# Kernel optimization log

Hardware: AMD Instinct MI355X
Metric: run time of the kernel (lower is better)

## Reference

```python
import jax, jax.numpy as jnp
import numpy as np

B, L, D_MODEL, H = 4, 4096, 1024, 16
HD = D_MODEL // H
EPS = 1e-6


def setup_inputs() -> dict:
    key = jax.random.key(0)
    ks = jax.random.split(key, 5)
    s = 1.0 / np.sqrt(D_MODEL)
    return {
        "x": jax.random.normal(ks[0], (B, L, D_MODEL), dtype=jnp.float32),
        "Wq": jax.random.normal(ks[1], (D_MODEL, D_MODEL), dtype=jnp.float32) * s,
        "bq": jnp.zeros((D_MODEL,), jnp.float32),
        "Wk": jax.random.normal(ks[2], (D_MODEL, D_MODEL), dtype=jnp.float32) * s,
        "bk": jnp.zeros((D_MODEL,), jnp.float32),
        "Wv": jax.random.normal(ks[3], (D_MODEL, D_MODEL), dtype=jnp.float32) * s,
        "bv": jnp.zeros((D_MODEL,), jnp.float32),
        "Wo": jax.random.normal(ks[4], (D_MODEL, D_MODEL), dtype=jnp.float32) * s,
        "bo": jnp.zeros((D_MODEL,), jnp.float32),
    }


def _heads(y):
    # (B, L, d_model) -> (B, H, L, head_dim)
    b, l, _ = y.shape
    return jnp.transpose(y.reshape(b, l, H, HD), (0, 2, 1, 3))


def reference(x, Wq, bq, Wk, bk, Wv, bv, Wo, bo):
    b, l, _ = x.shape
    q = jax.nn.sigmoid(_heads(x @ Wq + bq))  # kernel feature map
    k = jax.nn.sigmoid(_heads(x @ Wk + bk))
    v = _heads(x @ Wv + bv)

    sink_incoming = 1.0 / jnp.einsum('bhld,bhd->bhl', q + EPS, k.sum(axis=2) + EPS)
    source_outgoing = 1.0 / jnp.einsum('bhld,bhd->bhl', k + EPS, q.sum(axis=2) + EPS)
    conserved_sink = jnp.einsum(
        'bhld,bhd->bhl', q + EPS,
        (k * source_outgoing[..., None]).sum(axis=2) + EPS)
    conserved_source = jnp.einsum(
        'bhld,bhd->bhl', k + EPS,
        (q * sink_incoming[..., None]).sum(axis=2) + EPS)
    conserved_source = jnp.clip(conserved_source, -1.0, 1.0)

    sink_allocation = jax.nn.sigmoid(conserved_sink * (float(l) / float(l)))
    source_competition = jax.nn.softmax(conserved_source, axis=-1) * float(l)

    # linear attention: kv state (B,H,HD,HD) then apply to queries
    kv = jnp.einsum('bhld,bhlm->bhdm', k, v * source_competition[..., None])
    out = jnp.einsum('bhld,bhdm->bhlm', q * sink_incoming[..., None], kv)
    out = out * sink_allocation[..., None]

    out = jnp.transpose(out, (0, 2, 1, 3)).reshape(b, l, D_MODEL)
    # dropout is identity at inference
    return out @ Wo + bo
```

## Files before the change

### kernel.cpp

```cpp
#include <hip/hip_runtime.h>
#include <hip/hip_bf16.h>
#include <stdint.h>

#define SEQ    4096
#define DMODEL 1024
#define NHEAD  16
#define HDIM   64
#define NBATCH 4
#define NBH    (NBATCH*NHEAD)
#define MTOK   (NBATCH*SEQ)
#define FEPS   1e-6f
#define PLANE  16777216u

typedef float f32x4 __attribute__((ext_vector_type(4)));
typedef short bf16x8 __attribute__((ext_vector_type(8)));

#define XB_OFF    0u
#define WQKV_OFF  33554432u
#define WO_OFF    39845888u
#define QKV_OFF   41943040u
#define AOB_OFF   142606336u
#define ST_OFF    176160768u
#define KSUM_OFF  (ST_OFF)
#define QSUM_OFF  (ST_OFF + 16384u)
#define QSI_OFF   (ST_OFF + 32768u)
#define KSO_OFF   (ST_OFF + 49152u)
#define ESUM_OFF  (ST_OFF + 65536u)
#define SI_OFF    (ST_OFF + 81920u)
#define SA_OFF    (SI_OFF + 1048576u)
#define KVF_OFF   (SA_OFF + 1048576u)
#define KVP_OFF   (KVF_OFF + 1048576u)

#define S_VMCNT(N) asm volatile("s_waitcnt vmcnt(" #N ")" ::: "memory")
#define BARRIER() do { __builtin_amdgcn_s_barrier(); asm volatile("" ::: "memory"); } while (0)

__device__ __forceinline__ unsigned short f2bf(float f) {
  __hip_bfloat16 h = __float2bfloat16(f);
  unsigned short u; __builtin_memcpy(&u, &h, 2); return u;
}
__device__ __forceinline__ float bf2f(unsigned short u) {
  union { unsigned u; float f; } x; x.u = ((unsigned)u) << 16; return x.f;
}
__device__ __forceinline__ void decode8(uint4 r, float* o) {
  o[0] = bf2f((unsigned short)(r.x & 0xffffu)); o[1] = bf2f((unsigned short)(r.x >> 16));
  o[2] = bf2f((unsigned short)(r.y & 0xffffu)); o[3] = bf2f((unsigned short)(r.y >> 16));
  o[4] = bf2f((unsigned short)(r.z & 0xffffu)); o[5] = bf2f((unsigned short)(r.z >> 16));
  o[6] = bf2f((unsigned short)(r.w & 0xffffu)); o[7] = bf2f((unsigned short)(r.w >> 16));
}
__device__ __forceinline__ void gll(const unsigned short* g, unsigned short* l) {
  __builtin_amdgcn_global_load_lds((const __attribute__((address_space(1))) void*)g,
      (__attribute__((address_space(3))) void*)l, 16, 0, 0);
}

__global__ __launch_bounds__(256) void conv_all_k(const float* __restrict__ x,
                                                  const float* __restrict__ Wq, const float* __restrict__ Wk,
                                                  const float* __restrict__ Wv, const float* __restrict__ Wo,
                                                  unsigned short* __restrict__ xb,
                                                  unsigned short* __restrict__ Wqkvt,
                                                  unsigned short* __restrict__ Wot) {
  const int bx = blockIdx.x;
  if (bx < 1024) {
    __shared__ float tile[64][65];
    const int z = bx >> 8, tl = bx & 255;
    const float* W = (z == 0) ? Wq : (z == 1) ? Wk : (z == 2) ? Wv : Wo;
    unsigned short* dst = (z < 3) ? (Wqkvt + (size_t)z * 1024u * 1024u) : Wot;
    const int n0 = (tl & 15) * 64, k0 = (tl >> 4) * 64;
    const int tx = threadIdx.x & 63, ty = threadIdx.x >> 6;
    for (int i = ty; i < 64; i += 4)
      tile[i][tx] = W[(size_t)(k0 + i) * 1024 + n0 + tx];
    __syncthreads();
    for (int i = ty; i < 64; i += 4)
      dst[(size_t)(n0 + i) * 1024 + k0 + tx] = f2bf(tile[tx][i]);
  } else {
    const int n = MTOK * DMODEL;
    int i = ((bx - 1024) * 256 + threadIdx.x) * 4;
    const int stride = (gridDim.x - 1024) * 256 * 4;
    for (; i < n; i += stride) {
      float4 v = *(const float4*)(x + i);
      ushort4 o;
      o.x = f2bf(v.x); o.y = f2bf(v.y); o.z = f2bf(v.z); o.w = f2bf(v.w);
      *(ushort4*)(xb + i) = o;
    }
  }
}

template <int MODE>
__global__ __launch_bounds__(512, 2) void gemm8p(const unsigned short* __restrict__ A,
                                                 const unsigned short* __restrict__ Bt,
                                                 const float* __restrict__ b0,
                                                 const float* __restrict__ b1,
                                                 const float* __restrict__ b2,
                                                 float* __restrict__ qsum_g,
                                                 float* __restrict__ ksum_g,
                                                 void* __restrict__ C, int Ndim) {
  constexpr int Kd = 1024;
  constexpr int NT = Kd >> 6;
  __shared__ unsigned short sm[8 * 8192];
  const int tid = threadIdx.x;
  const int wid = tid >> 6, lane = tid & 63;
  const int wr = wid >> 2, wc = wid & 3;

  const int gx = gridDim.x;
  const int nwg = gx * gridDim.y;
  int wg = blockIdx.y * gx + blockIdx.x;
  wg = (wg & 7) * (nwg >> 3) + (wg >> 3);
  const int n0 = (wg % gx) * 256, m0 = (wg / gx) * 256;

  const int rl = lane & 15, kob = (lane >> 4) << 4;
  const int xs2 = (rl & 7) << 3;
  const int ca0 = (kob >> 1) ^ xs2;
  const int ca1 = (32 + (kob >> 1)) ^ xs2;
  const int brow0 = (wc & 1) * 64;
  const unsigned short* ArA = sm + wr * 8192 + rl * 64 + ca0;
  const unsigned short* ArB = sm + wr * 8192 + rl * 64 + ca1;
  const unsigned short* BrA = sm + (2 + (wc >> 1)) * 8192 + (brow0 + rl) * 64 + ca0;
  const unsigned short* BrB = sm + (2 + (wc >> 1)) * 8192 + (brow0 + rl) * 64 + ca1;

  const int srow = tid >> 3;
  const int scol = (((tid & 7) * 16) ^ ((srow & 7) << 4)) >> 1;
  const unsigned short* gA0 = A + (size_t)(m0 + srow) * Kd + scol;
  const unsigned short* gA1 = gA0 + 64 * Kd;
  const unsigned short* gA2 = gA0 + 128 * Kd;
  const unsigned short* gA3 = gA0 + 192 * Kd;
  const unsigned short* gB0 = Bt + (size_t)(n0 + srow) * Kd + scol;
  const unsigned short* gB1 = gB0 + 64 * Kd;
  const unsigned short* gB2 = gB0 + 128 * Kd;
  const unsigned short* gB3 = gB0 + 192 * Kd;
  unsigned short* ldst = sm + tid * 8;

  f32x4 acc[8][4];
#pragma unroll
  for (int i = 0; i < 8; ++i)
#pragma unroll
    for (int j = 0; j < 4; ++j) acc[i][j] = (f32x4){0.f, 0.f, 0.f, 0.f};

#define STG(g0, g1, R, T) do { \
    gll((g0) + (T) * 64, ldst + (R) * 8192); \
    gll((g1) + (T) * 64, ldst + (R) * 8192 + 4096); } while (0)

  STG(gA0, gA1, 0, 0); STG(gA2, gA3, 1, 0);
  STG(gB0, gB1, 2, 0); STG(gB2, gB3, 3, 0);
  STG(gA0, gA1, 4, 1); STG(gA2, gA3, 5, 1);
  S_VMCNT(4);
  BARRIER();

#define KBODY(U, BUF) do { \
    constexpr int BO = (BUF) * 32768; \
    bf16x8 a0[4][2], a1[4][2], b01[2][2], b23[2][2]; \
    _Pragma("unroll") for (int m = 0; m < 4; ++m) { \
      a0[m][0] = *(const bf16x8*)(ArA + BO + m * 1024); \
      a0[m][1] = *(const bf16x8*)(ArB + BO + m * 1024); } \
    _Pragma("unroll") for (int n = 0; n < 2; ++n) { \
      b01[n][0] = *(const bf16x8*)(BrA + BO + n * 1024); \
      b01[n][1] = *(const bf16x8*)(BrB + BO + n * 1024); } \
    if ((U) + 1 < NT) STG(gB0, gB1, (!(BUF)) * 4 + 2, (U) + 1); \
    BARRIER(); \
    __builtin_amdgcn_s_setprio(1); \
    _Pragma("unroll") for (int m = 0; m < 4; ++m) \
      _Pragma("unroll") for (int n = 0; n < 2; ++n) { \
        acc[m][n] = __builtin_amdgcn_mfma_f32_16x16x32_bf16(a0[m][0], b01[n][0], acc[m][n], 0, 0, 0); \
        acc[m][n] = __builtin_amdgcn_mfma_f32_16x16x32_bf16(a0[m][1], b01[n][1], acc[m][n], 0, 0, 0); } \
    __builtin_amdgcn_s_setprio(0); \
    BARRIER(); \
    _Pragma("unroll") for (int m = 0; m < 4; ++m) { \
      a1[m][0] = *(const bf16x8*)(ArA + BO + 4096 + m * 1024); \
      a1[m][1] = *(const bf16x8*)(ArB + BO + 4096 + m * 1024); } \
    if ((U) + 1 < NT) STG(gB2, gB3, (!(BUF)) * 4 + 3, (U) + 1); \
    BARRIER(); \
    __builtin_amdgcn_s_setprio(1); \
    _Pragma("unroll") for (int m = 0; m < 4; ++m) \
      _Pragma("unroll") for (int n = 0; n < 2; ++n) { \
        acc[4 + m][n] = __builtin_amdgcn_mfma_f32_16x16x32_bf16(a1[m][0], b01[n][0], acc[4 + m][n], 0, 0, 0); \
        acc[4 + m][n] = __builtin_amdgcn_mfma_f32_16x16x32_bf16(a1[m][1], b01[n][1], acc[4 + m][n], 0, 0, 0); } \
    __builtin_amdgcn_s_setprio(0); \
    BARRIER(); \
    _Pragma("unroll") for (int n = 0; n < 2; ++n) { \
      b23[n][0] = *(const bf16x8*)(BrA + BO + (2 + n) * 1024); \
      b23[n][1] = *(const bf16x8*)(BrB + BO + (2 + n) * 1024); } \
    if ((U) + 2 < NT) STG(gA0, gA1, (BUF) * 4, (U) + 2); \
    BARRIER(); \
    __builtin_amdgcn_s_setprio(1); \
    _Pragma("unroll") for (int m = 0; m < 4; ++m) \
      _Pragma("unroll") for (int n = 0; n < 2; ++n) { \
        acc[4 + m][2 + n] = __builtin_amdgcn_mfma_f32_16x16x32_bf16(a1[m][0], b23[n][0], acc[4 + m][2 + n], 0, 0, 0); \
        acc[4 + m][2 + n] = __builtin_amdgcn_mfma_f32_16x16x32_bf16(a1[m][1], b23[n][1], acc[4 + m][2 + n], 0, 0, 0); } \
    __builtin_amdgcn_s_setprio(0); \
    BARRIER(); \
    if ((U) + 2 < NT) STG(gA2, gA3, (BUF) * 4 + 1, (U) + 2); \
    BARRIER(); \
    __builtin_amdgcn_s_setprio(1); \
    _Pragma("unroll") for (int m = 0; m < 4; ++m) \
      _Pragma("unroll") for (int n = 0; n < 2; ++n) { \
        acc[m][2 + n] = __builtin_amdgcn_mfma_f32_16x16x32_bf16(a0[m][0], b23[n][0], acc[m][2 + n], 0, 0, 0); \
        acc[m][2 + n] = __builtin_amdgcn_mfma_f32_16x16x32_bf16(a0[m][1], b23[n][1], acc[m][2 + n], 0, 0, 0); } \
    __builtin_amdgcn_s_setprio(0); \
    if ((U) + 2 < NT) { S_VMCNT(4); } else { S_VMCNT(0); } \
    BARRIER(); \
  } while (0)

  for (int u = 0; u < NT; u += 2) {
    KBODY(u, 0);
    KBODY(u + 1, 1);
  }
#undef KBODY
#undef STG

  const int cr = (lane >> 4) * 4, cc = lane & 15;
  float cs[4] = {0.f, 0.f, 0.f, 0.f};
#pragma unroll
  for (int m = 0; m < 8; ++m)
#pragma unroll
    for (int n = 0; n < 4; ++n)
#pragma unroll
      for (int rr = 0; rr < 4; ++rr) {
        const int gr = m0 + wr * 128 + m * 16 + cr + rr;
        const int gc = n0 + wc * 64 + n * 16 + cc;
        float v = acc[m][n][rr];
        if (MODE == 0) {
          const float bias = (gc < 1024) ? b0[gc] : ((gc < 2048) ? b1[gc - 1024] : b2[gc - 2048]);
          v += bias;
          if (gc < 2048) v = 1.f / (1.f + __expf(-v));
          cs[n] += v;
          const size_t addr = (size_t)(gc >> 10) * PLANE +
                              ((size_t)(((gr >> 12) << 4) | ((gc >> 6) & 15)) * 4096 + (gr & 4095)) * 64 +
                              (gc & 63);
          ((unsigned short*)C)[addr] = f2bf(v);
        } else {
          v += b0[gc];
          ((float*)C)[(size_t)gr * Ndim + gc] = v;
        }
      }
  if (MODE == 0 && n0 < 2048) {
#pragma unroll
    for (int n = 0; n < 4; ++n) {
      cs[n] += __shfl_xor(cs[n], 16);
      cs[n] += __shfl_xor(cs[n], 32);
    }
    if (lane < 16) {
      const int b = m0 >> 12;
#pragma unroll
      for (int n = 0; n < 4; ++n) {
        const int gc = n0 + wc * 64 + n * 16 + lane;
        const int h = (gc & 1023) >> 6, d = gc & 63;
        float* tgt = (gc < 1024) ? qsum_g : ksum_g;
        atomicAdd(&tgt[((b << 4) + h) * 64 + d], cs[n]);
      }
    }
  }
}

__global__ __launch_bounds__(256) void flow1_k(const unsigned short* __restrict__ Qp,
                                               const unsigned short* __restrict__ Kp,
                                               const float* __restrict__ ksum, const float* __restrict__ qsum,
                                               float* __restrict__ si, float* __restrict__ qsi,
                                               float* __restrict__ kso) {
  const int bh = blockIdx.x >> 3, c = blockIdx.x & 7;
  const int w = threadIdx.x >> 6, lane = threadIdx.x & 63;
  const float ks = ksum[bh * 64 + lane] + FEPS;
  const float qs = qsum[bh * 64 + lane] + FEPS;
  const size_t hb = (size_t)bh * 262144 + lane;
  float qsi_acc = 0.f, kso_acc = 0.f;
  const int l0 = c * 512 + w * 128;
  for (int l = l0; l < l0 + 128; l += 4) {
    float qv[4], kvv[4], dq[4], dk[4];
#pragma unroll
    for (int u = 0; u < 4; ++u) {
      const size_t off = hb + (size_t)(l + u) * 64;
      qv[u] = bf2f(Qp[off]);
      kvv[u] = bf2f(Kp[off]);
      dq[u] = (qv[u] + FEPS) * ks;
      dk[u] = (kvv[u] + FEPS) * qs;
    }
#pragma unroll
    for (int m = 1; m < 64; m <<= 1)
#pragma unroll
      for (int u = 0; u < 4; ++u) { dq[u] += __shfl_xor(dq[u], m); dk[u] += __shfl_xor(dk[u], m); }
#pragma unroll
    for (int u = 0; u < 4; ++u) {
      const float siv = 1.f / dq[u], sov = 1.f / dk[u];
      if (lane == 0) si[(size_t)bh * SEQ + l + u] = siv;
      qsi_acc += qv[u] * siv;
      kso_acc += kvv[u] * sov;
    }
  }
  atomicAdd(&qsi[bh * 64 + lane], qsi_acc);
  atomicAdd(&kso[bh * 64 + lane], kso_acc);
}

__global__ __launch_bounds__(256) void flow2kv_k(const unsigned short* __restrict__ Qp,
                                                 const unsigned short* __restrict__ Kp,
                                                 const unsigned short* __restrict__ Vp,
                                                 const float* __restrict__ qsi, const float* __restrict__ kso,
                                                 float* __restrict__ sa, float* __restrict__ esum,
                                                 float* __restrict__ kvp) {
  const int bh = blockIdx.x >> 3, c = blockIdx.x & 7;
  __shared__ float eel[512];
  __shared__ float kch[32][64];
  __shared__ float vch[32][64];
  const int t = threadIdx.x;
  const int w = t >> 6, lane = t & 63;
  const size_t hb = (size_t)bh * 262144;

  {
    const float kov = kso[bh * 64 + lane] + FEPS;
    const float qiv = qsi[bh * 64 + lane] + FEPS;
    const size_t base = hb + lane;
    float es = 0.f;
    const int l0 = c * 512 + w * 128;
    for (int l = l0; l < l0 + 128; l += 4) {
      float ds[4], dr[4];
#pragma unroll
      for (int u = 0; u < 4; ++u) {
        const size_t off = base + (size_t)(l + u) * 64;
        ds[u] = (bf2f(Qp[off]) + FEPS) * kov;
        dr[u] = (bf2f(Kp[off]) + FEPS) * qiv;
      }
#pragma unroll
      for (int m = 1; m < 64; m <<= 1)
#pragma unroll
        for (int u = 0; u < 4; ++u) { ds[u] += __shfl_xor(ds[u], m); dr[u] += __shfl_xor(dr[u], m); }
#pragma unroll
      for (int u = 0; u < 4; ++u) {
        const float sig = 1.f / (1.f + __expf(-ds[u]));
        const float cse = fminf(1.f, fmaxf(-1.f, dr[u]));
        const float e = __expf(cse);
        if (lane == 0) { sa[(size_t)bh * SEQ + l + u] = sig; eel[l - c * 512 + u] = e; }
        es += e;
      }
    }
    if (lane == 0) atomicAdd(&esum[bh], es);
  }
  __syncthreads();

  const int sl = t >> 3, sd = (t & 7) * 8;
  const int d1 = (t >> 4) * 4, d2 = (t & 15) * 4;
  float acc[4][4] = {};
  for (int ch = 0; ch < 16; ++ch) {
    const int lloc = ch * 32 + sl;
    const size_t off = hb + (size_t)(c * 512 + lloc) * 64 + sd;
    const uint4 kr = *(const uint4*)(Kp + off);
    const uint4 vr = *(const uint4*)(Vp + off);
    const float cmp = eel[lloc];
    float kd[8], vd[8];
    decode8(kr, kd); decode8(vr, vd);
    __syncthreads();
    *(f32x4*)&kch[sl][sd]     = (f32x4){kd[0], kd[1], kd[2], kd[3]};
    *(f32x4*)&kch[sl][sd + 4] = (f32x4){kd[4], kd[5], kd[6], kd[7]};
    *(f32x4*)&vch[sl][sd]     = (f32x4){vd[0] * cmp, vd[1] * cmp, vd[2] * cmp, vd[3] * cmp};
    *(f32x4*)&vch[sl][sd + 4] = (f32x4){vd[4] * cmp, vd[5] * cmp, vd[6] * cmp, vd[7] * cmp};
    __syncthreads();
    for (int l = 0; l < 32; ++l) {
      const f32x4 ka = *(const f32x4*)&kch[l][d1];
      const f32x4 vb = *(const f32x4*)&vch[l][d2];
#pragma unroll
      for (int i = 0; i < 4; ++i)
#pragma unroll
        for (int j = 0; j < 4; ++j) acc[i][j] += ka[i] * vb[j];
    }
    __syncthreads();
  }
  float* dst = kvp + (size_t)blockIdx.x * 4096;
#pragma unroll
  for (int i = 0; i < 4; ++i)
    *(f32x4*)&dst[(d1 + i) * 64 + d2] = (f32x4){acc[i][0], acc[i][1], acc[i][2], acc[i][3]};
}

__global__ __launch_bounds__(256) void kvred_k(const float* __restrict__ kvp,
                                               const float* __restrict__ esum,
                                               float* __restrict__ kvf) {
  const int idx = blockIdx.x * 256 + threadIdx.x;
  const int bh = idx >> 12, e = idx & 4095;
  const float Ls = 4096.f / esum[bh];
  float s = 0.f;
#pragma unroll
  for (int cN = 0; cN < 8; ++cN) s += kvp[((size_t)(bh * 8 + cN) << 12) + e];
  kvf[idx] = s * Ls;
}

__global__ __launch_bounds__(256) void outk_k(const unsigned short* __restrict__ Qp,
                                              const float* __restrict__ kvf, const float* __restrict__ si,
                                              const float* __restrict__ sa,
                                              unsigned short* __restrict__ AOb) {
  const int bh = blockIdx.x >> 4, lc = blockIdx.x & 15;
  const int b = bh >> 4, h = bh & 15;
  __shared__ unsigned short kvT[4096];
  const int t = threadIdx.x;
  const int w = t >> 6, lane = t & 63;
  for (int i = t; i < 4096; i += 256) {
    const int dd = i >> 6, d = i & 63;
    kvT[d * 64 + (dd ^ ((d & 7) << 3))] = f2bf(kvf[(size_t)bh * 4096 + i]);
  }
  __syncthreads();

  const int rl = lane & 15, g = lane >> 4;
  const size_t hb = (size_t)bh * 262144;
  const int l0 = lc * 256 + w * 64;

  bf16x8 a[4][2], bf[4][2];
#pragma unroll
  for (int m = 0; m < 4; ++m) {
    const size_t q0 = hb + (size_t)(l0 + m * 16 + rl) * 64 + g * 8;
    a[m][0] = *(const bf16x8*)(Qp + q0);
    a[m][1] = *(const bf16x8*)(Qp + q0 + 32);
  }
#pragma unroll
  for (int n = 0; n < 4; ++n) {
    const int r = n * 16 + rl;
    const int sw = (r & 7) << 3;
    bf[n][0] = *(const bf16x8*)(kvT + r * 64 + ((g * 8) ^ sw));
    bf[n][1] = *(const bf16x8*)(kvT + r * 64 + ((32 + g * 8) ^ sw));
  }
  f32x4 acc[4][4];
#pragma unroll
  for (int i = 0; i < 4; ++i)
#pragma unroll
    for (int j = 0; j < 4; ++j) acc[i][j] = (f32x4){0.f, 0.f, 0.f, 0.f};
#pragma unroll
  for (int m = 0; m < 4; ++m)
#pragma unroll
    for (int n = 0; n < 4; ++n) {
      acc[m][n] = __builtin_amdgcn_mfma_f32_16x16x32_bf16(a[m][0], bf[n][0], acc[m][n], 0, 0, 0);
      acc[m][n] = __builtin_amdgcn_mfma_f32_16x16x32_bf16(a[m][1], bf[n][1], acc[m][n], 0, 0, 0);
    }

  const int cr = (lane >> 4) * 4, cc = lane & 15;
#pragma unroll
  for (int m = 0; m < 4; ++m)
#pragma unroll
    for (int rr = 0; rr < 4; ++rr) {
      const int l = l0 + m * 16 + cr + rr;
      const size_t sidx = (size_t)bh * SEQ + l;
      const float sc = si[sidx] * sa[sidx];
      unsigned short* orow = AOb + (size_t)(b * SEQ + l) * 1024 + h * 64 + cc;
#pragma unroll
      for (int n = 0; n < 4; ++n)
        orow[n * 16] = f2bf(acc[m][n][rr] * sc);
    }
}

extern "C" void kernel_launch(void* const* d_in, const int* in_sizes, int n_in,
                              void* d_out, int out_size, void* d_ws, size_t ws_size,
                              hipStream_t stream) {
  const float* x  = (const float*)d_in[0];
  const float* Wq = (const float*)d_in[1];
  const float* bq = (const float*)d_in[2];
  const float* Wk = (const float*)d_in[3];
  const float* bk = (const float*)d_in[4];
  const float* Wv = (const float*)d_in[5];
  const float* bv = (const float*)d_in[6];
  const float* Wo = (const float*)d_in[7];
  const float* bo = (const float*)d_in[8];
  char* ws = (char*)d_ws;
  unsigned short* Xb    = (unsigned short*)(ws + XB_OFF);
  unsigned short* Wqkvt = (unsigned short*)(ws + WQKV_OFF);
  unsigned short* Wot   = (unsigned short*)(ws + WO_OFF);
  unsigned short* QKV   = (unsigned short*)(ws + QKV_OFF);
  unsigned short* AOb   = (unsigned short*)(ws + AOB_OFF);
  unsigned short* Qp = QKV;
  unsigned short* Kp = QKV + PLANE;
  unsigned short* Vp = QKV + 2 * PLANE;
  float* ksum = (float*)(ws + KSUM_OFF);
  float* qsum = (float*)(ws + QSUM_OFF);
  float* qsi  = (float*)(ws + QSI_OFF);
  float* kso  = (float*)(ws + KSO_OFF);
  float* esum = (float*)(ws + ESUM_OFF);
  float* si   = (float*)(ws + SI_OFF);
  float* sa   = (float*)(ws + SA_OFF);
  float* kvf  = (float*)(ws + KVF_OFF);
  float* kvp  = (float*)(ws + KVP_OFF);

  (void)hipMemsetAsync(ws + ST_OFF, 0, 81920, stream);
  conv_all_k<<<3072, 256, 0, stream>>>(x, Wq, Wk, Wv, Wo, Xb, Wqkvt, Wot);
  gemm8p<0><<<dim3(12, 64), 512, 0, stream>>>(Xb, Wqkvt, bq, bk, bv, qsum, ksum, (void*)QKV, 3072);
  flow1_k<<<NBH * 8, 256, 0, stream>>>(Qp, Kp, ksum, qsum, si, qsi, kso);
  flow2kv_k<<<NBH * 8, 256, 0, stream>>>(Qp, Kp, Vp, qsi, kso, sa, esum, kvp);
  kvred_k<<<1024, 256, 0, stream>>>(kvp, esum, kvf);
  outk_k<<<NBH * 16, 256, 0, stream>>>(Qp, kvf, si, sa, AOb);
  gemm8p<1><<<dim3(4, 64), 512, 0, stream>>>(AOb, Wot, bo, nullptr, nullptr, nullptr, nullptr, d_out, 1024);
}
```

Measured before the change: 335.3 us.

## Vectorize flow kernels' row reductions and fold KV partial reduction into output kernel

flow1_k and the first phase of flow2kv_k now load 8 bf16 values per lane with 16-byte loads, so 8 lanes cover one 64-wide row and each wave processes 8 rows at a time. This replaces scalar 2-byte loads and full 64-lane shuffle reductions with a 3-step shuffle, plus a final cross-row shuffle before the atomics. The separate kvred_k launch is removed. outk_k now sums the 8 KV partials itself and applies the esum scale, which drops one kernel launch and the kvf round trip through memory. The cost is that each of the 16 outk blocks per head repeats the partial-sum work.

```diff
diff --git a/kernel.cpp b/kernel.cpp
--- a/kernel.cpp
+++ b/kernel.cpp
@@ -28,8 +28,7 @@
 #define ESUM_OFF  (ST_OFF + 65536u)
 #define SI_OFF    (ST_OFF + 81920u)
 #define SA_OFF    (SI_OFF + 1048576u)
-#define KVF_OFF   (SA_OFF + 1048576u)
-#define KVP_OFF   (KVF_OFF + 1048576u)
+#define KVP_OFF   (SA_OFF + 1048576u)
 
 #define S_VMCNT(N) asm volatile("s_waitcnt vmcnt(" #N ")" ::: "memory")
 #define BARRIER() do { __builtin_amdgcn_s_barrier(); asm volatile("" ::: "memory"); } while (0)
@@ -255,36 +254,49 @@
                                                float* __restrict__ si, float* __restrict__ qsi,
                                                float* __restrict__ kso) {
   const int bh = blockIdx.x >> 3, c = blockIdx.x & 7;
-  const int w = threadIdx.x >> 6, lane = threadIdx.x & 63;
-  const float ks = ksum[bh * 64 + lane] + FEPS;
-  const float qs = qsum[bh * 64 + lane] + FEPS;
-  const size_t hb = (size_t)bh * 262144 + lane;
-  float qsi_acc = 0.f, kso_acc = 0.f;
-  const int l0 = c * 512 + w * 128;
-  for (int l = l0; l < l0 + 128; l += 4) {
-    float qv[4], kvv[4], dq[4], dk[4];
-#pragma unroll
-    for (int u = 0; u < 4; ++u) {
-      const size_t off = hb + (size_t)(l + u) * 64;
-      qv[u] = bf2f(Qp[off]);
-      kvv[u] = bf2f(Kp[off]);
-      dq[u] = (qv[u] + FEPS) * ks;
-      dk[u] = (kvv[u] + FEPS) * qs;
-    }
-#pragma unroll
-    for (int m = 1; m < 64; m <<= 1)
-#pragma unroll
-      for (int u = 0; u < 4; ++u) { dq[u] += __shfl_xor(dq[u], m); dk[u] += __shfl_xor(dk[u], m); }
-#pragma unroll
-    for (int u = 0; u < 4; ++u) {
-      const float siv = 1.f / dq[u], sov = 1.f / dk[u];
-      if (lane == 0) si[(size_t)bh * SEQ + l + u] = siv;
-      qsi_acc += qv[u] * siv;
-      kso_acc += kvv[u] * sov;
-    }
-  }
-  atomicAdd(&qsi[bh * 64 + lane], qsi_acc);
-  atomicAdd(&kso[bh * 64 + lane], kso_acc);
+  const int t = threadIdx.x;
+  const int w = t >> 6, lane = t & 63;
+  const int r = lane >> 3, dg = lane & 7;
+  const size_t hb = (size_t)bh * 262144;
+  float ksv[8], qsv[8];
+#pragma unroll
+  for (int j = 0; j < 8; ++j) {
+    ksv[j] = ksum[bh * 64 + dg * 8 + j] + FEPS;
+    qsv[j] = qsum[bh * 64 + dg * 8 + j] + FEPS;
+  }
+  float qsi_acc[8] = {}, kso_acc[8] = {};
+  const int l0w = c * 512 + w * 128;
+  for (int l4 = 0; l4 < 128; l4 += 8) {
+    const int l = l0w + l4 + r;
+    const size_t off = hb + (size_t)l * 64 + dg * 8;
+    const uint4 qr = *(const uint4*)(Qp + off);
+    const uint4 kr = *(const uint4*)(Kp + off);
+    float qd[8], kd[8];
+    decode8(qr, qd); decode8(kr, kd);
+    float dq = 0.f, dk = 0.f;
+#pragma unroll
+    for (int j = 0; j < 8; ++j) { dq += (qd[j] + FEPS) * ksv[j]; dk += (kd[j] + FEPS) * qsv[j]; }
+#pragma unroll
+    for (int m = 1; m < 8; m <<= 1) { dq += __shfl_xor(dq, m); dk += __shfl_xor(dk, m); }
+    const float siv = 1.f / dq, sov = 1.f / dk;
+    if (dg == 0) si[(size_t)bh * SEQ + l] = siv;
+#pragma unroll
+    for (int j = 0; j < 8; ++j) { qsi_acc[j] += qd[j] * siv; kso_acc[j] += kd[j] * sov; }
+  }
+#pragma unroll
+  for (int m = 8; m < 64; m <<= 1)
+#pragma unroll
+    for (int j = 0; j < 8; ++j) {
+      qsi_acc[j] += __shfl_xor(qsi_acc[j], m);
+      kso_acc[j] += __shfl_xor(kso_acc[j], m);
+    }
+  if (lane < 8) {
+#pragma unroll
+    for (int j = 0; j < 8; ++j) {
+      atomicAdd(&qsi[bh * 64 + lane * 8 + j], qsi_acc[j]);
+      atomicAdd(&kso[bh * 64 + lane * 8 + j], kso_acc[j]);
+    }
+  }
 }
 
 __global__ __launch_bounds__(256) void flow2kv_k(const unsigned short* __restrict__ Qp,
@@ -302,32 +314,38 @@
   const size_t hb = (size_t)bh * 262144;
 
   {
-    const float kov = kso[bh * 64 + lane] + FEPS;
-    const float qiv = qsi[bh * 64 + lane] + FEPS;
-    const size_t base = hb + lane;
+    const int r = lane >> 3, dg = lane & 7;
+    float kov[8], qiv[8];
+#pragma unroll
+    for (int j = 0; j < 8; ++j) {
+      kov[j] = kso[bh * 64 + dg * 8 + j] + FEPS;
+      qiv[j] = qsi[bh * 64 + dg * 8 + j] + FEPS;
+    }
     float es = 0.f;
-    const int l0 = c * 512 + w * 128;
-    for (int l = l0; l < l0 + 128; l += 4) {
-      float ds[4], dr[4];
-#pragma unroll
-      for (int u = 0; u < 4; ++u) {
-        const size_t off = base + (size_t)(l + u) * 64;
-        ds[u] = (bf2f(Qp[off]) + FEPS) * kov;
-        dr[u] = (bf2f(Kp[off]) + FEPS) * qiv;
-      }
-#pragma unroll
-      for (int m = 1; m < 64; m <<= 1)
-#pragma unroll
-        for (int u = 0; u < 4; ++u) { ds[u] += __shfl_xor(ds[u], m); dr[u] += __shfl_xor(dr[u], m); }
-#pragma unroll
-      for (int u = 0; u < 4; ++u) {
-        const float sig = 1.f / (1.f + __expf(-ds[u]));
-        const float cse = fminf(1.f, fmaxf(-1.f, dr[u]));
-        const float e = __expf(cse);
-        if (lane == 0) { sa[(size_t)bh * SEQ + l + u] = sig; eel[l - c * 512 + u] = e; }
+    const int l0w = c * 512 + w * 128;
+    for (int l4 = 0; l4 < 128; l4 += 8) {
+      const int l = l0w + l4 + r;
+      const size_t off = hb + (size_t)l * 64 + dg * 8;
+      const uint4 qr = *(const uint4*)(Qp + off);
+      const uint4 kr = *(const uint4*)(Kp + off);
+      float qd[8], kd[8];
+      decode8(qr, qd); decode8(kr, kd);
+      float ds = 0.f, dr = 0.f;
+#pragma unroll
+      for (int j = 0; j < 8; ++j) { ds += (qd[j] + FEPS) * kov[j]; dr += (kd[j] + FEPS) * qiv[j]; }
+#pragma unroll
+      for (int m = 1; m < 8; m <<= 1) { ds += __shfl_xor(ds, m); dr += __shfl_xor(dr, m); }
+      const float sig = 1.f / (1.f + __expf(-ds));
+      const float cse = fminf(1.f, fmaxf(-1.f, dr));
+      const float e = __expf(cse);
+      if (dg == 0) {
+        sa[(size_t)bh * SEQ + l] = sig;
+        eel[w * 128 + l4 + r] = e;
         es += e;
       }
     }
+#pragma unroll
+    for (int m = 8; m < 64; m <<= 1) es += __shfl_xor(es, m);
     if (lane == 0) atomicAdd(&esum[bh], es);
   }
   __syncthreads();
@@ -365,30 +383,22 @@
     *(f32x4*)&dst[(d1 + i) * 64 + d2] = (f32x4){acc[i][0], acc[i][1], acc[i][2], acc[i][3]};
 }
 
-__global__ __launch_bounds__(256) void kvred_k(const float* __restrict__ kvp,
-                                               const float* __restrict__ esum,
-                                               float* __restrict__ kvf) {
-  const int idx = blockIdx.x * 256 + threadIdx.x;
-  const int bh = idx >> 12, e = idx & 4095;
-  const float Ls = 4096.f / esum[bh];
-  float s = 0.f;
-#pragma unroll
-  for (int cN = 0; cN < 8; ++cN) s += kvp[((size_t)(bh * 8 + cN) << 12) + e];
-  kvf[idx] = s * Ls;
-}
-
 __global__ __launch_bounds__(256) void outk_k(const unsigned short* __restrict__ Qp,
-                                              const float* __restrict__ kvf, const float* __restrict__ si,
-                                              const float* __restrict__ sa,
+                                              const float* __restrict__ kvp, const float* __restrict__ esum,
+                                              const float* __restrict__ si, const float* __restrict__ sa,
                                               unsigned short* __restrict__ AOb) {
   const int bh = blockIdx.x >> 4, lc = blockIdx.x & 15;
   const int b = bh >> 4, h = bh & 15;
   __shared__ unsigned short kvT[4096];
   const int t = threadIdx.x;
   const int w = t >> 6, lane = t & 63;
+  const float Ls = 4096.f / esum[bh];
   for (int i = t; i < 4096; i += 256) {
+    float s = 0.f;
+#pragma unroll
+    for (int cN = 0; cN < 8; ++cN) s += kvp[((size_t)(bh * 8 + cN)) * 4096 + i];
     const int dd = i >> 6, d = i & 63;
-    kvT[d * 64 + (dd ^ ((d & 7) << 3))] = f2bf(kvf[(size_t)bh * 4096 + i]);
+    kvT[d * 64 + (dd ^ ((d & 7) << 3))] = f2bf(s * Ls);
   }
   __syncthreads();
 
@@ -466,7 +476,6 @@
   float* esum = (float*)(ws + ESUM_OFF);
   float* si   = (float*)(ws + SI_OFF);
   float* sa   = (float*)(ws + SA_OFF);
-  float* kvf  = (float*)(ws + KVF_OFF);
   float* kvp  = (float*)(ws + KVP_OFF);
 
   (void)hipMemsetAsync(ws + ST_OFF, 0, 81920, stream);
@@ -474,7 +483,6 @@
   gemm8p<0><<<dim3(12, 64), 512, 0, stream>>>(Xb, Wqkvt, bq, bk, bv, qsum, ksum, (void*)QKV, 3072);
   flow1_k<<<NBH * 8, 256, 0, stream>>>(Qp, Kp, ksum, qsum, si, qsi, kso);
   flow2kv_k<<<NBH * 8, 256, 0, stream>>>(Qp, Kp, Vp, qsi, kso, sa, esum, kvp);
-  kvred_k<<<1024, 256, 0, stream>>>(kvp, esum, kvf);
-  outk_k<<<NBH * 16, 256, 0, stream>>>(Qp, kvf, si, sa, AOb);
+  outk_k<<<NBH * 16, 256, 0, stream>>>(Qp, kvp, esum, si, sa, AOb);
   gemm8p<1><<<dim3(4, 64), 512, 0, stream>>>(AOb, Wot, bo, nullptr, nullptr, nullptr, nullptr, d_out, 1024);
 }
```

Result: faster. 297.6 us (-11.2%).
